# Kernel tuning notes

Measured on AMD Instinct MI355X. Metric: run time of the kernel, lower is better.

Reference implementation:

```python
import math
import jax, jax.numpy as jnp
import numpy as np

B, T, D, H = 2, 2048, 1024, 16
HD = D // H  # 64


def _rope(x, freq_cis):
    # x: (B, T, H, HD); freq_cis: (1, T, 1, HD//2) complex
    Bx, Tx, Hx, Dx = x.shape
    xc = jax.lax.complex(x[..., 0::2], x[..., 1::2])
    xr = xc * freq_cis
    return jnp.stack([xr.real, xr.imag], axis=-1).reshape(Bx, Tx, Hx, Dx)


def setup_inputs() -> dict:
    key = jax.random.key(0)
    ks = jax.random.split(key, 10)
    x = jax.random.normal(ks[0], (B, T, D), dtype=jnp.float32)
    # causal mask, broadcast over batch and heads
    mask = jnp.tril(jnp.ones((T, T), dtype=bool))[None, None]
    # RoPE angles: theta_j = 10000^{-2j/HD}, angle[t, j] = t * theta_j
    inv_freq = 1.0 / (10000.0 ** (jnp.arange(0, HD, 2, dtype=jnp.float32) / HD))  # (HD/2,)
    freqs = (jnp.arange(T, dtype=jnp.float32)[:, None] * inv_freq[None, :])[None, :, None, :]  # (1,T,1,HD/2)
    s = 1.0 / math.sqrt(D)
    Wq = jax.random.normal(ks[1], (D, D), dtype=jnp.float32) * s
    bq = jnp.zeros((D,), dtype=jnp.float32)
    Wk = jax.random.normal(ks[2], (D, D), dtype=jnp.float32) * s
    bk = jnp.zeros((D,), dtype=jnp.float32)
    Wv = jax.random.normal(ks[3], (D, D), dtype=jnp.float32) * s
    bv = jnp.zeros((D,), dtype=jnp.float32)
    Wo = jax.random.normal(ks[4], (D, D), dtype=jnp.float32) * s
    bo = jnp.zeros((D,), dtype=jnp.float32)
    return {"x": x, "mask": mask, "freqs": freqs,
            "Wq": Wq, "bq": bq, "Wk": Wk, "bk": bk,
            "Wv": Wv, "bv": bv, "Wo": Wo, "bo": bo}


def reference(x, mask, freqs, Wq, bq, Wk, bk, Wv, bv, Wo, bo):
    Bx, Tx, Dx = x.shape
    freq_cis = jax.lax.complex(jnp.cos(freqs), jnp.sin(freqs))  # (1,T,1,HD/2)
    q = (x @ Wq + bq).reshape(Bx, Tx, H, HD)
    k = (x @ Wk + bk).reshape(Bx, Tx, H, HD)
    v = (x @ Wv + bv).reshape(Bx, Tx, H, HD)
    q = _rope(q, freq_cis)
    k = _rope(k, freq_cis)
    # (B, H, T, HD)
    q = q.transpose(0, 2, 1, 3)
    k = k.transpose(0, 2, 1, 3)
    v = v.transpose(0, 2, 1, 3)
    attn = jnp.einsum('bhqd,bhkd->bhqk', q, k) / math.sqrt(HD)
    attn = jnp.where(mask, attn, -1e9)
    probs = jax.nn.softmax(attn, axis=-1)  # dropout is identity (deterministic=True)
    out = jnp.einsum('bhqk,bhkd->bhqd', probs, v)
    out = out.transpose(0, 2, 1, 3).reshape(Bx, Tx, Dx)
    return out @ Wo + bo
```

## Files before the change

### kernel.cpp

```cpp
#include <hip/hip_runtime.h>
#include <cstdint>
#include <cstddef>

typedef __bf16 bf16x8 __attribute__((ext_vector_type(8)));
typedef float  f32x4  __attribute__((ext_vector_type(4)));

#define DEV __device__ __forceinline__

DEV unsigned short f2bf(float f) {
  union { float f; unsigned u; } x; x.f = f;
  unsigned r = x.u + 0x7fffu + ((x.u >> 16) & 1u);
  return (unsigned short)(r >> 16);
}

DEV void gl_lds16(const void* g, void* l) {
  __builtin_amdgcn_global_load_lds((const __attribute__((address_space(1))) void*)g,
                                   (__attribute__((address_space(3))) void*)l, 16, 0, 0);
}

DEV bf16x8 lds_frag(const void* base, int byteoff) {
  return *reinterpret_cast<const bf16x8*>(reinterpret_cast<const char*>(base) + byteoff);
}

DEV f32x4 MFMA(bf16x8 a, bf16x8 b, f32x4 c) {
  return __builtin_amdgcn_mfma_f32_16x16x32_bf16(a, b, c, 0, 0, 0);
}

__global__ __launch_bounds__(256) void k_cast_x(const float* __restrict__ x,
                                                unsigned short* __restrict__ xb) {
  int i = (blockIdx.x * 256 + threadIdx.x) * 8;
  float4 a = *(const float4*)(x + i);
  float4 b = *(const float4*)(x + i + 4);
  uint4 o;
  o.x = (unsigned)f2bf(a.x) | ((unsigned)f2bf(a.y) << 16);
  o.y = (unsigned)f2bf(a.z) | ((unsigned)f2bf(a.w) << 16);
  o.z = (unsigned)f2bf(b.x) | ((unsigned)f2bf(b.y) << 16);
  o.w = (unsigned)f2bf(b.z) | ((unsigned)f2bf(b.w) << 16);
  *reinterpret_cast<uint4*>(xb + i) = o;
}

__global__ __launch_bounds__(256) void k_trans_w(const float* __restrict__ Wq, const float* __restrict__ Wk,
                                                 const float* __restrict__ Wv, const float* __restrict__ Wo,
                                                 unsigned short* __restrict__ WT) {
  __shared__ float tile[32][33];
  int z = blockIdx.z;
  const float* W = (z == 0) ? Wq : ((z == 1) ? Wk : ((z == 2) ? Wv : Wo));
  unsigned short* out = WT + ((size_t)z << 20);
  int x = threadIdx.x, y = threadIdx.y;
  int gx = blockIdx.x * 32 + x;
  int gy = blockIdx.y * 32;
#pragma unroll
  for (int i = 0; i < 4; ++i) tile[y + i * 8][x] = W[(size_t)(gy + y + i * 8) * 1024 + gx];
  __syncthreads();
#pragma unroll
  for (int i = 0; i < 4; ++i)
    out[(size_t)(blockIdx.x * 32 + y + i * 8) * 1024 + gy + x] = f2bf(tile[x][y + i * 8]);
}

__global__ __launch_bounds__(256) void k_cs(const float* __restrict__ freqs, float* __restrict__ tab) {
  int i = blockIdx.x * 256 + threadIdx.x;
  float a = freqs[i];
  float s, c;
  sincosf(a, &s, &c);
  ((float2*)tab)[i] = make_float2(c, s);
}

__global__ __launch_bounds__(256) void k_qkv(const unsigned short* __restrict__ xb,
                                             const unsigned short* __restrict__ WT,
                                             const float* __restrict__ bq,
                                             const float* __restrict__ bk,
                                             const float* __restrict__ bv,
                                             const float* __restrict__ tab,
                                             unsigned short* __restrict__ qws,
                                             unsigned short* __restrict__ kws,
                                             unsigned short* __restrict__ vtb) {
  __shared__ __align__(16) unsigned short As[2][128 * 32];
  __shared__ __align__(16) unsigned short Bs[2][128 * 32];
  int t = threadIdx.x, w = t >> 6, l = t & 63;
  int z = blockIdx.z;
  int n0 = blockIdx.x * 128, m0 = blockIdx.y * 128;
  const unsigned short* Wz = WT + ((size_t)z << 20);
  int wm = w >> 1, wn = w & 1;
  f32x4 zero4 = {0.f, 0.f, 0.f, 0.f};
  f32x4 acc[4][4];
#pragma unroll
  for (int i = 0; i < 4; ++i)
#pragma unroll
    for (int j = 0; j < 4; ++j) acc[i][j] = zero4;

  int aoff[4], boff[4];
#pragma unroll
  for (int i = 0; i < 4; ++i) {
    aoff[i] = ((wm * 64 + i * 16 + (l & 15)) * 32 + ((l >> 4) * 8)) * 2;
    boff[i] = ((wn * 64 + i * 16 + (l & 15)) * 32 + ((l >> 4) * 8)) * 2;
  }
  int r0 = t >> 2, c0 = t & 3;

#define QSTAGE(k0v, buf) do { \
    char* la = (char*)As + (buf) * 8192 + w * 1024; \
    char* lb = (char*)Bs + (buf) * 8192 + w * 1024; \
    const char* ga0 = (const char*)xb + ((size_t)(m0 + r0) * 1024 + (k0v) + c0 * 8) * 2; \
    const char* ga1 = (const char*)xb + ((size_t)(m0 + 64 + r0) * 1024 + (k0v) + c0 * 8) * 2; \
    const char* gb0 = (const char*)Wz + ((size_t)(n0 + r0) * 1024 + (k0v) + c0 * 8) * 2; \
    const char* gb1 = (const char*)Wz + ((size_t)(n0 + 64 + r0) * 1024 + (k0v) + c0 * 8) * 2; \
    gl_lds16(ga0, la); gl_lds16(ga1, la + 4096); \
    gl_lds16(gb0, lb); gl_lds16(gb1, lb + 4096); \
  } while (0)

  QSTAGE(0, 0);
  asm volatile("s_waitcnt vmcnt(0)" ::: "memory");
  __syncthreads();
  for (int k0 = 0; k0 < 1024; k0 += 32) {
    int cur = (k0 >> 5) & 1;
    if (k0 + 32 < 1024) QSTAGE(k0 + 32, cur ^ 1);
    const char* Ab = (const char*)As + cur * 8192;
    const char* Bb = (const char*)Bs + cur * 8192;
    bf16x8 af[4], bfr[4];
#pragma unroll
    for (int i = 0; i < 4; ++i) af[i] = lds_frag(Ab, aoff[i]);
#pragma unroll
    for (int i = 0; i < 4; ++i) bfr[i] = lds_frag(Bb, boff[i]);
#pragma unroll
    for (int i = 0; i < 4; ++i)
#pragma unroll
      for (int jn = 0; jn < 4; ++jn) acc[i][jn] = MFMA(af[i], bfr[jn], acc[i][jn]);
    asm volatile("s_waitcnt vmcnt(0)" ::: "memory");
    __syncthreads();
  }
#undef QSTAGE

  int nb = n0 + wn * 64, mb = m0 + wm * 64;
  if (z == 2) {
#pragma unroll
    for (int i = 0; i < 4; ++i)
#pragma unroll
      for (int jn = 0; jn < 4; ++jn) {
        int n = nb + jn * 16 + (l & 15);
        float bsv = bv[n];
        int hh = n >> 6, hd = n & 63;
        int m0j = mb + i * 16 + ((l >> 4) << 2);
        int bb = m0j >> 11, tt = m0j & 2047;
        ushort4 pk;
        pk.x = f2bf(acc[i][jn][0] + bsv);
        pk.y = f2bf(acc[i][jn][1] + bsv);
        pk.z = f2bf(acc[i][jn][2] + bsv);
        pk.w = f2bf(acc[i][jn][3] + bsv);
        *(ushort4*)&vtb[(((size_t)(bb * 16 + hh) * 64 + hd) * 2048) + tt] = pk;
      }
  } else {
    const float* bias = (z == 0) ? bq : bk;
    unsigned short* outp = (z == 0) ? qws : kws;
#pragma unroll
    for (int i = 0; i < 4; ++i)
#pragma unroll
      for (int jn = 0; jn < 4; ++jn) {
        int n = nb + jn * 16 + (l & 15);
        float bsv = bias[n];
        int hd = n & 63;
#pragma unroll
        for (int j = 0; j < 4; ++j) {
          int m = mb + i * 16 + ((l >> 4) << 2) + j;
          float val = acc[i][jn][j] + bsv;
          int trow = m & 2047;
          float2 cs = ((const float2*)tab)[trow * 32 + (hd >> 1)];
          float part = __shfl_xor(val, 1);
          val = (hd & 1) ? fmaf(part, cs.y, val * cs.x) : fmaf(val, cs.x, -part * cs.y);
          outp[(size_t)m * 1024 + n] = f2bf(val);
        }
      }
  }
}

DEV void attn_strip(const bf16x8 (&qf)[2], f32x4 (&po)[4], float (&m_run)[4], float (&l_run)[4],
                    bool diag, const char* Kb, const char* Vb, unsigned short* pw, int w, int l) {
  const float KL2E = 0.18033688011112042f;
  f32x4 zero4 = {0.f, 0.f, 0.f, 0.f};
  f32x4 ps[4];
#pragma unroll
  for (int bn = 0; bn < 4; ++bn) ps[bn] = zero4;
  __builtin_amdgcn_s_setprio(1);
#pragma unroll
  for (int ks = 0; ks < 2; ++ks)
#pragma unroll
    for (int bn = 0; bn < 4; ++bn) {
      int row = bn * 16 + (l & 15);
      bf16x8 kf = lds_frag(Kb, row * 128 + (((ks * 4 + (l >> 4)) ^ (row & 7)) << 4));
      ps[bn] = MFMA(qf[ks], kf, ps[bn]);
    }
  __builtin_amdgcn_s_setprio(0);
  if (diag) {
#pragma unroll
    for (int bn = 0; bn < 4; ++bn) {
      int kv = bn * 16 + (l & 15);
#pragma unroll
      for (int j = 0; j < 4; ++j) {
        int r = ((l >> 4) << 2) + j;
        if (kv > w * 16 + r) ps[bn][j] = -1e30f;
      }
    }
  }
  float rm[4];
#pragma unroll
  for (int j = 0; j < 4; ++j)
    rm[j] = fmaxf(fmaxf(ps[0][j], ps[1][j]), fmaxf(ps[2][j], ps[3][j]));
#pragma unroll
  for (int off = 1; off < 16; off <<= 1)
#pragma unroll
    for (int j = 0; j < 4; ++j) rm[j] = fmaxf(rm[j], __shfl_xor(rm[j], off));
  float alpha[4], rs[4];
#pragma unroll
  for (int j = 0; j < 4; ++j) {
    float mn = fmaxf(m_run[j], rm[j]);
    alpha[j] = exp2f((m_run[j] - mn) * KL2E);
    m_run[j] = mn;
    rs[j] = 0.f;
  }
#pragma unroll
  for (int bn = 0; bn < 4; ++bn)
#pragma unroll
    for (int j = 0; j < 4; ++j) {
      float p = exp2f((ps[bn][j] - m_run[j]) * KL2E);
      ps[bn][j] = p;
      rs[j] += p;
    }
#pragma unroll
  for (int off = 1; off < 16; off <<= 1)
#pragma unroll
    for (int j = 0; j < 4; ++j) rs[j] += __shfl_xor(rs[j], off);
#pragma unroll
  for (int j = 0; j < 4; ++j) l_run[j] = l_run[j] * alpha[j] + rs[j];
#pragma unroll
  for (int hf = 0; hf < 4; ++hf)
#pragma unroll
    for (int j = 0; j < 4; ++j) po[hf][j] *= alpha[j];
#pragma unroll
  for (int bn = 0; bn < 4; ++bn)
#pragma unroll
    for (int j = 0; j < 4; ++j) {
      int r = ((l >> 4) << 2) + j, c = bn * 16 + (l & 15);
      pw[r * 64 + (((c >> 3) ^ (r & 7)) << 3) + (c & 7)] = f2bf(ps[bn][j]);
    }
  asm volatile("" ::: "memory");
  __builtin_amdgcn_s_setprio(1);
#pragma unroll
  for (int ks = 0; ks < 2; ++ks) {
    int prow = l & 15;
    bf16x8 pa = lds_frag(pw, prow * 128 + (((ks * 4 + (l >> 4)) ^ (prow & 7)) << 4));
#pragma unroll
    for (int hf = 0; hf < 4; ++hf) {
      int vrow = hf * 16 + (l & 15);
      bf16x8 vf = lds_frag(Vb, vrow * 128 + (((ks * 4 + (l >> 4)) ^ (vrow & 7)) << 4));
      po[hf] = MFMA(pa, vf, po[hf]);
    }
  }
  __builtin_amdgcn_s_setprio(0);
  asm volatile("" ::: "memory");
}

__global__ __launch_bounds__(256) void k_attn(const unsigned short* __restrict__ qb,
                                              const unsigned short* __restrict__ kb,
                                              const unsigned short* __restrict__ vtb,
                                              unsigned short* __restrict__ ab) {
  __shared__ __align__(16) unsigned short Ks[2][64 * 64];
  __shared__ __align__(16) unsigned short Vts[2][64 * 64];
  __shared__ __align__(16) unsigned short PsA[4 * 16 * 64];
  __shared__ __align__(16) unsigned short PsB[4 * 16 * 64];
  int t = threadIdx.x, w = t >> 6, l = t & 63;
  int lid = blockIdx.x;
  int xcd = lid & 7, rest = lid >> 3;
  int bh = xcd + 8 * (rest & 3);
  int pi = rest >> 2;
  int qtA = pi, qtB = 31 - pi;
  int b = bh >> 4, h = bh & 15;

  bf16x8 qfA[2], qfB[2];
  {
    int mA = b * 2048 + qtA * 64 + w * 16 + (l & 15);
    const char* qp = (const char*)qb + ((size_t)mA * 1024 + h * 64 + ((l >> 4) * 8)) * 2;
    qfA[0] = *(const bf16x8*)qp;
    qfA[1] = *(const bf16x8*)(qp + 64);
    int mB = b * 2048 + qtB * 64 + w * 16 + (l & 15);
    const char* qp2 = (const char*)qb + ((size_t)mB * 1024 + h * 64 + ((l >> 4) * 8)) * 2;
    qfB[0] = *(const bf16x8*)qp2;
    qfB[1] = *(const bf16x8*)(qp2 + 64);
  }
  f32x4 zero4 = {0.f, 0.f, 0.f, 0.f};
  f32x4 poA[4], poB[4];
  float mA_[4], lA_[4], mB_[4], lB_[4];
#pragma unroll
  for (int i = 0; i < 4; ++i) {
    poA[i] = zero4; poB[i] = zero4;
    mA_[i] = -1e30f; lA_[i] = 0.f;
    mB_[i] = -1e30f; lB_[i] = 0.f;
  }
  unsigned short* pwA = PsA + w * 1024;
  unsigned short* pwB = PsB + w * 1024;
  int r0 = t >> 3, s0 = t & 7, lc0 = s0 ^ (r0 & 7);
  int r1 = 32 + r0;
  const char* kbase = (const char*)kb + ((size_t)(b * 2048) * 1024 + h * 64) * 2;
  const char* vbase = (const char*)vtb + ((size_t)bh * 64) * 2048 * 2;

#define ASTAGE(jt, buf) do { \
    char* lk = (char*)Ks + (buf) * 8192 + w * 1024; \
    char* lv = (char*)Vts + (buf) * 8192 + w * 1024; \
    const char* gk0 = kbase + ((size_t)((jt) * 64 + r0) * 1024) * 2 + lc0 * 16; \
    const char* gk1 = kbase + ((size_t)((jt) * 64 + r1) * 1024) * 2 + lc0 * 16; \
    const char* gv0 = vbase + (size_t)r0 * 4096 + (jt) * 128 + lc0 * 16; \
    const char* gv1 = vbase + (size_t)r1 * 4096 + (jt) * 128 + lc0 * 16; \
    gl_lds16(gk0, lk); gl_lds16(gk1, lk + 4096); \
    gl_lds16(gv0, lv); gl_lds16(gv1, lv + 4096); \
  } while (0)

  ASTAGE(0, 0);
  asm volatile("s_waitcnt vmcnt(0)" ::: "memory");
  __syncthreads();
  for (int jt = 0; jt <= qtB; ++jt) {
    int cur = jt & 1;
    if (jt < qtB) ASTAGE(jt + 1, cur ^ 1);
    const char* Kb = (const char*)Ks + cur * 8192;
    const char* Vb = (const char*)Vts + cur * 8192;
    attn_strip(qfB, poB, mB_, lB_, jt == qtB, Kb, Vb, pwB, w, l);
    if (jt <= qtA) attn_strip(qfA, poA, mA_, lA_, jt == qtA, Kb, Vb, pwA, w, l);
    asm volatile("s_waitcnt vmcnt(0)" ::: "memory");
    __syncthreads();
  }
#undef ASTAGE

#pragma unroll
  for (int s = 0; s < 2; ++s) {
    f32x4* po = s ? poB : poA;
    float* lr = s ? lB_ : lA_;
    int qt = s ? qtB : qtA;
    float inv[4];
#pragma unroll
    for (int j = 0; j < 4; ++j) inv[j] = 1.0f / lr[j];
#pragma unroll
    for (int hf = 0; hf < 4; ++hf)
#pragma unroll
      for (int j = 0; j < 4; ++j) {
        int r = ((l >> 4) << 2) + j;
        int m = b * 2048 + qt * 64 + w * 16 + r;
        int col = h * 64 + hf * 16 + (l & 15);
        ab[(size_t)m * 1024 + col] = f2bf(po[hf][j] * inv[j]);
      }
  }
}

__global__ __launch_bounds__(256) void k_oproj(const unsigned short* __restrict__ ab,
                                               const unsigned short* __restrict__ WoT,
                                               const float* __restrict__ bo,
                                               float* __restrict__ out) {
  __shared__ __align__(16) unsigned short As[2][128 * 32];
  __shared__ __align__(16) unsigned short Bs[2][128 * 32];
  int t = threadIdx.x, w = t >> 6, l = t & 63;
  int n0 = blockIdx.x * 128, m0 = blockIdx.y * 128;
  int wm = w >> 1, wn = w & 1;
  f32x4 zero4 = {0.f, 0.f, 0.f, 0.f};
  f32x4 acc[4][4];
#pragma unroll
  for (int i = 0; i < 4; ++i)
#pragma unroll
    for (int j = 0; j < 4; ++j) acc[i][j] = zero4;
  int aoff[4], boff[4];
#pragma unroll
  for (int i = 0; i < 4; ++i) {
    aoff[i] = ((wm * 64 + i * 16 + (l & 15)) * 32 + ((l >> 4) * 8)) * 2;
    boff[i] = ((wn * 64 + i * 16 + (l & 15)) * 32 + ((l >> 4) * 8)) * 2;
  }
  int r0 = t >> 2, c0 = t & 3;

#define OSTAGE(k0v, buf) do { \
    char* la = (char*)As + (buf) * 8192 + w * 1024; \
    char* lb = (char*)Bs + (buf) * 8192 + w * 1024; \
    const char* ga0 = (const char*)ab + ((size_t)(m0 + r0) * 1024 + (k0v) + c0 * 8) * 2; \
    const char* ga1 = (const char*)ab + ((size_t)(m0 + 64 + r0) * 1024 + (k0v) + c0 * 8) * 2; \
    const char* gb0 = (const char*)WoT + ((size_t)(n0 + r0) * 1024 + (k0v) + c0 * 8) * 2; \
    const char* gb1 = (const char*)WoT + ((size_t)(n0 + 64 + r0) * 1024 + (k0v) + c0 * 8) * 2; \
    gl_lds16(ga0, la); gl_lds16(ga1, la + 4096); \
    gl_lds16(gb0, lb); gl_lds16(gb1, lb + 4096); \
  } while (0)

  OSTAGE(0, 0);
  asm volatile("s_waitcnt vmcnt(0)" ::: "memory");
  __syncthreads();
  for (int k0 = 0; k0 < 1024; k0 += 32) {
    int cur = (k0 >> 5) & 1;
    if (k0 + 32 < 1024) OSTAGE(k0 + 32, cur ^ 1);
    const char* Ab = (const char*)As + cur * 8192;
    const char* Bb = (const char*)Bs + cur * 8192;
    bf16x8 af[4], bfr[4];
#pragma unroll
    for (int i = 0; i < 4; ++i) af[i] = lds_frag(Ab, aoff[i]);
#pragma unroll
    for (int i = 0; i < 4; ++i) bfr[i] = lds_frag(Bb, boff[i]);
#pragma unroll
    for (int i = 0; i < 4; ++i)
#pragma unroll
      for (int jn = 0; jn < 4; ++jn) acc[i][jn] = MFMA(af[i], bfr[jn], acc[i][jn]);
    asm volatile("s_waitcnt vmcnt(0)" ::: "memory");
    __syncthreads();
  }
#undef OSTAGE

  int nb = n0 + wn * 64, mb = m0 + wm * 64;
#pragma unroll
  for (int i = 0; i < 4; ++i)
#pragma unroll
    for (int jn = 0; jn < 4; ++jn) {
      int n = nb + jn * 16 + (l & 15);
      float bsv = bo[n];
#pragma unroll
      for (int j = 0; j < 4; ++j) {
        int m = mb + i * 16 + ((l >> 4) << 2) + j;
        out[(size_t)m * 1024 + n] = acc[i][jn][j] + bsv;
      }
    }
}

extern "C" void kernel_launch(void* const* d_in, const int* in_sizes, int n_in,
                              void* d_out, int out_size, void* d_ws, size_t ws_size,
                              hipStream_t stream) {
  const float* x     = (const float*)d_in[0];
  const float* freqs = (const float*)d_in[2];
  const float* Wq    = (const float*)d_in[3];
  const float* bq    = (const float*)d_in[4];
  const float* Wk    = (const float*)d_in[5];
  const float* bk    = (const float*)d_in[6];
  const float* Wv    = (const float*)d_in[7];
  const float* bv    = (const float*)d_in[8];
  const float* Wo    = (const float*)d_in[9];
  const float* bo    = (const float*)d_in[10];

  char* ws = (char*)d_ws;
  unsigned short* xb  = (unsigned short*)(ws);
  unsigned short* WT  = (unsigned short*)(ws + ((size_t)8 << 20));
  unsigned short* qb  = (unsigned short*)(ws + ((size_t)16 << 20));
  unsigned short* kb  = (unsigned short*)(ws + ((size_t)24 << 20));
  unsigned short* vtb = (unsigned short*)(ws + ((size_t)40 << 20));
  unsigned short* ab  = (unsigned short*)(ws + ((size_t)48 << 20));
  float*          tab = (float*)(ws + ((size_t)56 << 20));

  k_cast_x<<<2048, 256, 0, stream>>>(x, xb);
  k_trans_w<<<dim3(32, 32, 4), dim3(32, 8), 0, stream>>>(Wq, Wk, Wv, Wo, WT);
  k_cs<<<256, 256, 0, stream>>>(freqs, tab);
  k_qkv<<<dim3(8, 32, 3), 256, 0, stream>>>(xb, WT, bq, bk, bv, tab, qb, kb, vtb);
  k_attn<<<dim3(512), 256, 0, stream>>>(qb, kb, vtb, ab);
  k_oproj<<<dim3(8, 32), 256, 0, stream>>>(ab, WT + ((size_t)3 << 20), bo, (float*)d_out);
}
```

Baseline: 273.6 us.

## Fold softmax scale into Wq, lazy rescaling, MFMA row sums, separate V transpose

Pre-scales Wq and bq by log2(e)/sqrt(D) so scores arrive in the exp2 domain, and uses raw v_exp_f32. The online softmax now rescales only when some score exceeds the running max by more than a threshold, and the running sum is computed by an MFMA against a ones vector instead of shuffle reductions. K and V fragments are loaded from LDS once per tile and shared by both query strips. The V transpose moves out of the QKV epilogue into a new kernel, which adds a launch and an extra pass over V. Lazy rescaling can let exponent values grow large, which risks precision loss.

```diff
diff --git a/kernel.cpp b/kernel.cpp
--- a/kernel.cpp
+++ b/kernel.cpp
@@ -13,6 +13,12 @@
   return (unsigned short)(r >> 16);
 }
 
+DEV float fexp2(float x) {
+  float r;
+  asm("v_exp_f32 %0, %1" : "=v"(r) : "v"(x));
+  return r;
+}
+
 DEV void gl_lds16(const void* g, void* l) {
   __builtin_amdgcn_global_load_lds((const __attribute__((address_space(1))) void*)g,
                                    (__attribute__((address_space(3))) void*)l, 16, 0, 0);
@@ -25,6 +31,8 @@
 DEV f32x4 MFMA(bf16x8 a, bf16x8 b, f32x4 c) {
   return __builtin_amdgcn_mfma_f32_16x16x32_bf16(a, b, c, 0, 0, 0);
 }
+
+#define KL2E 0.18033688011112042f
 
 __global__ __launch_bounds__(256) void k_cast_x(const float* __restrict__ x,
                                                 unsigned short* __restrict__ xb) {
@@ -45,6 +53,7 @@
   __shared__ float tile[32][33];
   int z = blockIdx.z;
   const float* W = (z == 0) ? Wq : ((z == 1) ? Wk : ((z == 2) ? Wv : Wo));
+  float scl = (z == 0) ? KL2E : 1.0f;
   unsigned short* out = WT + ((size_t)z << 20);
   int x = threadIdx.x, y = threadIdx.y;
   int gx = blockIdx.x * 32 + x;
@@ -54,7 +63,7 @@
   __syncthreads();
 #pragma unroll
   for (int i = 0; i < 4; ++i)
-    out[(size_t)(blockIdx.x * 32 + y + i * 8) * 1024 + gy + x] = f2bf(tile[x][y + i * 8]);
+    out[(size_t)(blockIdx.x * 32 + y + i * 8) * 1024 + gy + x] = f2bf(tile[x][y + i * 8] * scl);
 }
 
 __global__ __launch_bounds__(256) void k_cs(const float* __restrict__ freqs, float* __restrict__ tab) {
@@ -73,7 +82,7 @@
                                              const float* __restrict__ tab,
                                              unsigned short* __restrict__ qws,
                                              unsigned short* __restrict__ kws,
-                                             unsigned short* __restrict__ vtb) {
+                                             unsigned short* __restrict__ vws) {
   __shared__ __align__(16) unsigned short As[2][128 * 32];
   __shared__ __align__(16) unsigned short Bs[2][128 * 32];
   int t = threadIdx.x, w = t >> 6, l = t & 63;
@@ -129,129 +138,133 @@
   }
 #undef QSTAGE
 
+  const float* bias = (z == 0) ? bq : ((z == 1) ? bk : bv);
+  unsigned short* outp = (z == 0) ? qws : ((z == 1) ? kws : vws);
+  float bscl = (z == 0) ? KL2E : 1.0f;
+  bool doRope = (z < 2);
   int nb = n0 + wn * 64, mb = m0 + wm * 64;
-  if (z == 2) {
-#pragma unroll
-    for (int i = 0; i < 4; ++i)
-#pragma unroll
-      for (int jn = 0; jn < 4; ++jn) {
-        int n = nb + jn * 16 + (l & 15);
-        float bsv = bv[n];
-        int hh = n >> 6, hd = n & 63;
-        int m0j = mb + i * 16 + ((l >> 4) << 2);
-        int bb = m0j >> 11, tt = m0j & 2047;
-        ushort4 pk;
-        pk.x = f2bf(acc[i][jn][0] + bsv);
-        pk.y = f2bf(acc[i][jn][1] + bsv);
-        pk.z = f2bf(acc[i][jn][2] + bsv);
-        pk.w = f2bf(acc[i][jn][3] + bsv);
-        *(ushort4*)&vtb[(((size_t)(bb * 16 + hh) * 64 + hd) * 2048) + tt] = pk;
-      }
-  } else {
-    const float* bias = (z == 0) ? bq : bk;
-    unsigned short* outp = (z == 0) ? qws : kws;
-#pragma unroll
-    for (int i = 0; i < 4; ++i)
-#pragma unroll
-      for (int jn = 0; jn < 4; ++jn) {
-        int n = nb + jn * 16 + (l & 15);
-        float bsv = bias[n];
-        int hd = n & 63;
-#pragma unroll
-        for (int j = 0; j < 4; ++j) {
-          int m = mb + i * 16 + ((l >> 4) << 2) + j;
-          float val = acc[i][jn][j] + bsv;
+#pragma unroll
+  for (int i = 0; i < 4; ++i) {
+#pragma unroll
+    for (int jn = 0; jn < 4; ++jn) {
+      int n = nb + jn * 16 + (l & 15);
+      float bsv = bias[n] * bscl;
+      int hd = n & 63;
+#pragma unroll
+      for (int j = 0; j < 4; ++j) {
+        int m = mb + i * 16 + ((l >> 4) << 2) + j;
+        float val = acc[i][jn][j] + bsv;
+        if (doRope) {
           int trow = m & 2047;
           float2 cs = ((const float2*)tab)[trow * 32 + (hd >> 1)];
           float part = __shfl_xor(val, 1);
           val = (hd & 1) ? fmaf(part, cs.y, val * cs.x) : fmaf(val, cs.x, -part * cs.y);
-          outp[(size_t)m * 1024 + n] = f2bf(val);
         }
+        ((__bf16*)outp)[(size_t)m * 1024 + n] = (__bf16)val;
       }
-  }
-}
-
-DEV void attn_strip(const bf16x8 (&qf)[2], f32x4 (&po)[4], float (&m_run)[4], float (&l_run)[4],
-                    bool diag, const char* Kb, const char* Vb, unsigned short* pw, int w, int l) {
-  const float KL2E = 0.18033688011112042f;
-  f32x4 zero4 = {0.f, 0.f, 0.f, 0.f};
+    }
+  }
+}
+
+__global__ __launch_bounds__(256) void k_vtrans(const unsigned short* __restrict__ vb,
+                                                unsigned short* __restrict__ vtb) {
+  __shared__ unsigned short vt[64 * 72];
+  int t = threadIdx.x;
+  int tt = blockIdx.x, bh = blockIdx.y;
+  int b = bh >> 4, h = bh & 15;
+  int row = t >> 2, ch = t & 3;
+  const char* src = (const char*)vb + (((size_t)(b * 2048 + tt * 64 + row) * 1024) + h * 64 + ch * 16) * 2;
+  uint4 v0 = *(const uint4*)src;
+  uint4 v1 = *(const uint4*)(src + 16);
+  const unsigned short* e0 = (const unsigned short*)&v0;
+  const unsigned short* e1 = (const unsigned short*)&v1;
+#pragma unroll
+  for (int i = 0; i < 8; ++i) vt[(ch * 16 + i) * 72 + row] = e0[i];
+#pragma unroll
+  for (int i = 0; i < 8; ++i) vt[(ch * 16 + 8 + i) * 72 + row] = e1[i];
+  __syncthreads();
+  int hd = t >> 2, c2 = t & 3;
+  uint4 o0 = *(const uint4*)&vt[hd * 72 + c2 * 16];
+  uint4 o1 = *(const uint4*)&vt[hd * 72 + c2 * 16 + 8];
+  char* dst = (char*)vtb + (((size_t)(bh * 64 + hd) * 2048) + tt * 64 + c2 * 16) * 2;
+  *(uint4*)dst = o0;
+  *(uint4*)(dst + 16) = o1;
+}
+
+DEV void attn_strip(const bf16x8 (&qf)[2], const bf16x8 (&kc)[2][4], const bf16x8 (&vc)[2][4],
+                    f32x4 (&po)[4], f32x4 &lsum, float (&m_run)[4],
+                    bool diag, unsigned short* pw, int w, int l) {
+  int hi = l >> 4, lo = l & 15;
+  f32x4 minit = {-m_run[0], -m_run[1], -m_run[2], -m_run[3]};
   f32x4 ps[4];
 #pragma unroll
-  for (int bn = 0; bn < 4; ++bn) ps[bn] = zero4;
+  for (int bn = 0; bn < 4; ++bn) ps[bn] = minit;
   __builtin_amdgcn_s_setprio(1);
 #pragma unroll
   for (int ks = 0; ks < 2; ++ks)
 #pragma unroll
-    for (int bn = 0; bn < 4; ++bn) {
-      int row = bn * 16 + (l & 15);
-      bf16x8 kf = lds_frag(Kb, row * 128 + (((ks * 4 + (l >> 4)) ^ (row & 7)) << 4));
-      ps[bn] = MFMA(qf[ks], kf, ps[bn]);
-    }
+    for (int bn = 0; bn < 4; ++bn) ps[bn] = MFMA(qf[ks], kc[ks][bn], ps[bn]);
   __builtin_amdgcn_s_setprio(0);
   if (diag) {
 #pragma unroll
     for (int bn = 0; bn < 4; ++bn) {
-      int kv = bn * 16 + (l & 15);
+      int kv = bn * 16 + lo;
 #pragma unroll
       for (int j = 0; j < 4; ++j) {
-        int r = ((l >> 4) << 2) + j;
+        int r = (hi << 2) + j;
         if (kv > w * 16 + r) ps[bn][j] = -1e30f;
       }
     }
   }
-  float rm[4];
-#pragma unroll
-  for (int j = 0; j < 4; ++j)
-    rm[j] = fmaxf(fmaxf(ps[0][j], ps[1][j]), fmaxf(ps[2][j], ps[3][j]));
-#pragma unroll
-  for (int off = 1; off < 16; off <<= 1)
-#pragma unroll
-    for (int j = 0; j < 4; ++j) rm[j] = fmaxf(rm[j], __shfl_xor(rm[j], off));
-  float alpha[4], rs[4];
-#pragma unroll
-  for (int j = 0; j < 4; ++j) {
-    float mn = fmaxf(m_run[j], rm[j]);
-    alpha[j] = exp2f((m_run[j] - mn) * KL2E);
-    m_run[j] = mn;
-    rs[j] = 0.f;
+  float t0 = fmaxf(fmaxf(ps[0][0], ps[0][1]), fmaxf(ps[0][2], ps[0][3]));
+  float t1 = fmaxf(fmaxf(ps[1][0], ps[1][1]), fmaxf(ps[1][2], ps[1][3]));
+  float t2 = fmaxf(fmaxf(ps[2][0], ps[2][1]), fmaxf(ps[2][2], ps[2][3]));
+  float t3 = fmaxf(fmaxf(ps[3][0], ps[3][1]), fmaxf(ps[3][2], ps[3][3]));
+  float tm = fmaxf(fmaxf(t0, t1), fmaxf(t2, t3));
+  if (__any(tm > 8.0f)) {
+    float rm[4];
+#pragma unroll
+    for (int j = 0; j < 4; ++j)
+      rm[j] = fmaxf(fmaxf(ps[0][j], ps[1][j]), fmaxf(ps[2][j], ps[3][j]));
+#pragma unroll
+    for (int off = 1; off < 16; off <<= 1)
+#pragma unroll
+      for (int j = 0; j < 4; ++j) rm[j] = fmaxf(rm[j], __shfl_xor(rm[j], off));
+    float d[4], al[4];
+#pragma unroll
+    for (int j = 0; j < 4; ++j) {
+      d[j] = fmaxf(rm[j], 0.f);
+      al[j] = fexp2(-d[j]);
+      m_run[j] += d[j];
+    }
+#pragma unroll
+    for (int bn = 0; bn < 4; ++bn)
+#pragma unroll
+      for (int j = 0; j < 4; ++j) ps[bn][j] -= d[j];
+#pragma unroll
+    for (int hf = 0; hf < 4; ++hf)
+#pragma unroll
+      for (int j = 0; j < 4; ++j) po[hf][j] *= al[j];
+#pragma unroll
+    for (int j = 0; j < 4; ++j) lsum[j] *= al[j];
   }
 #pragma unroll
   for (int bn = 0; bn < 4; ++bn)
 #pragma unroll
     for (int j = 0; j < 4; ++j) {
-      float p = exp2f((ps[bn][j] - m_run[j]) * KL2E);
-      ps[bn][j] = p;
-      rs[j] += p;
-    }
-#pragma unroll
-  for (int off = 1; off < 16; off <<= 1)
-#pragma unroll
-    for (int j = 0; j < 4; ++j) rs[j] += __shfl_xor(rs[j], off);
-#pragma unroll
-  for (int j = 0; j < 4; ++j) l_run[j] = l_run[j] * alpha[j] + rs[j];
-#pragma unroll
-  for (int hf = 0; hf < 4; ++hf)
-#pragma unroll
-    for (int j = 0; j < 4; ++j) po[hf][j] *= alpha[j];
-#pragma unroll
-  for (int bn = 0; bn < 4; ++bn)
-#pragma unroll
-    for (int j = 0; j < 4; ++j) {
-      int r = ((l >> 4) << 2) + j, c = bn * 16 + (l & 15);
-      pw[r * 64 + (((c >> 3) ^ (r & 7)) << 3) + (c & 7)] = f2bf(ps[bn][j]);
+      int r = (hi << 2) + j, c = bn * 16 + lo;
+      ((__bf16*)pw)[r * 64 + (((c >> 3) ^ (r & 7)) << 3) + (c & 7)] = (__bf16)fexp2(ps[bn][j]);
     }
   asm volatile("" ::: "memory");
+  __bf16 one = (__bf16)1.0f;
+  bf16x8 ones = {one, one, one, one, one, one, one, one};
   __builtin_amdgcn_s_setprio(1);
 #pragma unroll
   for (int ks = 0; ks < 2; ++ks) {
-    int prow = l & 15;
-    bf16x8 pa = lds_frag(pw, prow * 128 + (((ks * 4 + (l >> 4)) ^ (prow & 7)) << 4));
-#pragma unroll
-    for (int hf = 0; hf < 4; ++hf) {
-      int vrow = hf * 16 + (l & 15);
-      bf16x8 vf = lds_frag(Vb, vrow * 128 + (((ks * 4 + (l >> 4)) ^ (vrow & 7)) << 4));
-      po[hf] = MFMA(pa, vf, po[hf]);
-    }
+    bf16x8 pa = lds_frag(pw, lo * 128 + (((ks * 4 + hi) ^ (lo & 7)) << 4));
+#pragma unroll
+    for (int hf = 0; hf < 4; ++hf) po[hf] = MFMA(pa, vc[ks][hf], po[hf]);
+    lsum = MFMA(pa, ones, lsum);
   }
   __builtin_amdgcn_s_setprio(0);
   asm volatile("" ::: "memory");
@@ -272,26 +285,26 @@
   int pi = rest >> 2;
   int qtA = pi, qtB = 31 - pi;
   int b = bh >> 4, h = bh & 15;
+  int hi = l >> 4, lo = l & 15;
 
   bf16x8 qfA[2], qfB[2];
   {
-    int mA = b * 2048 + qtA * 64 + w * 16 + (l & 15);
-    const char* qp = (const char*)qb + ((size_t)mA * 1024 + h * 64 + ((l >> 4) * 8)) * 2;
+    int mA = b * 2048 + qtA * 64 + w * 16 + lo;
+    const char* qp = (const char*)qb + ((size_t)mA * 1024 + h * 64 + hi * 8) * 2;
     qfA[0] = *(const bf16x8*)qp;
     qfA[1] = *(const bf16x8*)(qp + 64);
-    int mB = b * 2048 + qtB * 64 + w * 16 + (l & 15);
-    const char* qp2 = (const char*)qb + ((size_t)mB * 1024 + h * 64 + ((l >> 4) * 8)) * 2;
+    int mB = b * 2048 + qtB * 64 + w * 16 + lo;
+    const char* qp2 = (const char*)qb + ((size_t)mB * 1024 + h * 64 + hi * 8) * 2;
     qfB[0] = *(const bf16x8*)qp2;
     qfB[1] = *(const bf16x8*)(qp2 + 64);
   }
   f32x4 zero4 = {0.f, 0.f, 0.f, 0.f};
-  f32x4 poA[4], poB[4];
-  float mA_[4], lA_[4], mB_[4], lB_[4];
+  f32x4 poA[4], poB[4], lsumA = zero4, lsumB = zero4;
+  float mA_[4], mB_[4];
 #pragma unroll
   for (int i = 0; i < 4; ++i) {
     poA[i] = zero4; poB[i] = zero4;
-    mA_[i] = -1e30f; lA_[i] = 0.f;
-    mB_[i] = -1e30f; lB_[i] = 0.f;
+    mA_[i] = 0.f;  mB_[i] = 0.f;
   }
   unsigned short* pwA = PsA + w * 1024;
   unsigned short* pwB = PsB + w * 1024;
@@ -319,8 +332,17 @@
     if (jt < qtB) ASTAGE(jt + 1, cur ^ 1);
     const char* Kb = (const char*)Ks + cur * 8192;
     const char* Vb = (const char*)Vts + cur * 8192;
-    attn_strip(qfB, poB, mB_, lB_, jt == qtB, Kb, Vb, pwB, w, l);
-    if (jt <= qtA) attn_strip(qfA, poA, mA_, lA_, jt == qtA, Kb, Vb, pwA, w, l);
+    bf16x8 kc[2][4], vc[2][4];
+#pragma unroll
+    for (int ks = 0; ks < 2; ++ks)
+#pragma unroll
+      for (int i = 0; i < 4; ++i) {
+        int row = i * 16 + lo;
+        kc[ks][i] = lds_frag(Kb, row * 128 + (((ks * 4 + hi) ^ (lo & 7)) << 4));
+        vc[ks][i] = lds_frag(Vb, row * 128 + (((ks * 4 + hi) ^ (lo & 7)) << 4));
+      }
+    attn_strip(qfB, kc, vc, poB, lsumB, mB_, jt == qtB, pwB, w, l);
+    if (jt <= qtA) attn_strip(qfA, kc, vc, poA, lsumA, mA_, jt == qtA, pwA, w, l);
     asm volatile("s_waitcnt vmcnt(0)" ::: "memory");
     __syncthreads();
   }
@@ -329,19 +351,19 @@
 #pragma unroll
   for (int s = 0; s < 2; ++s) {
     f32x4* po = s ? poB : poA;
-    float* lr = s ? lB_ : lA_;
+    f32x4 ls = s ? lsumB : lsumA;
     int qt = s ? qtB : qtA;
     float inv[4];
 #pragma unroll
-    for (int j = 0; j < 4; ++j) inv[j] = 1.0f / lr[j];
+    for (int j = 0; j < 4; ++j) inv[j] = 1.0f / ls[j];
 #pragma unroll
     for (int hf = 0; hf < 4; ++hf)
 #pragma unroll
       for (int j = 0; j < 4; ++j) {
-        int r = ((l >> 4) << 2) + j;
+        int r = (hi << 2) + j;
         int m = b * 2048 + qt * 64 + w * 16 + r;
-        int col = h * 64 + hf * 16 + (l & 15);
-        ab[(size_t)m * 1024 + col] = f2bf(po[hf][j] * inv[j]);
+        int col = h * 64 + hf * 16 + lo;
+        ((__bf16*)ab)[(size_t)m * 1024 + col] = (__bf16)(po[hf][j] * inv[j]);
       }
   }
 }
@@ -436,6 +458,7 @@
   unsigned short* WT  = (unsigned short*)(ws + ((size_t)8 << 20));
   unsigned short* qb  = (unsigned short*)(ws + ((size_t)16 << 20));
   unsigned short* kb  = (unsigned short*)(ws + ((size_t)24 << 20));
+  unsigned short* vb  = (unsigned short*)(ws + ((size_t)32 << 20));
   unsigned short* vtb = (unsigned short*)(ws + ((size_t)40 << 20));
   unsigned short* ab  = (unsigned short*)(ws + ((size_t)48 << 20));
   float*          tab = (float*)(ws + ((size_t)56 << 20));
@@ -443,7 +466,8 @@
   k_cast_x<<<2048, 256, 0, stream>>>(x, xb);
   k_trans_w<<<dim3(32, 32, 4), dim3(32, 8), 0, stream>>>(Wq, Wk, Wv, Wo, WT);
   k_cs<<<256, 256, 0, stream>>>(freqs, tab);
-  k_qkv<<<dim3(8, 32, 3), 256, 0, stream>>>(xb, WT, bq, bk, bv, tab, qb, kb, vtb);
+  k_qkv<<<dim3(8, 32, 3), 256, 0, stream>>>(xb, WT, bq, bk, bv, tab, qb, kb, vb);
+  k_vtrans<<<dim3(32, 32), 256, 0, stream>>>(vb, vtb);
   k_attn<<<dim3(512), 256, 0, stream>>>(qb, kb, vtb, ab);
   k_oproj<<<dim3(8, 32), 256, 0, stream>>>(ab, WT + ((size_t)3 << 20), bo, (float*)d_out);
 }
```

Result: faster. 246.7 us (-9.8%).
